# Performance work log

Measured on AMD Instinct MI355X. Metric: run time of the kernel, lower is better.

The kernel has to match this reference:

```python
import jax, jax.numpy as jnp
import numpy as np

N = 50000      # nodes
E = 640000     # edges
F_IN = 128     # in_channels
H = 128        # hidden / layer size
G = 64         # graphs in batch
OUT = 5        # classes


def _lin_init(key, fan_in, fan_out):
    s = 1.0 / np.sqrt(fan_in)
    kw, kb = jax.random.split(key)
    w = jax.random.uniform(kw, (fan_in, fan_out), jnp.float32, -s, s)
    b = jax.random.uniform(kb, (fan_out,), jnp.float32, -s, s)
    return w, b


def setup_inputs() -> dict:
    key = jax.random.key(0)
    ks = jax.random.split(key, 8)
    x = jax.random.normal(ks[0], (N, F_IN), jnp.float32)
    edge_index = jax.random.randint(ks[1], (2, E), 0, N, dtype=jnp.int64)
    # sorted graph assignment, every graph nonempty (sorted_randint-style)
    batch = (jnp.arange(N, dtype=jnp.int64) * G) // N
    c0w1, c0b1 = _lin_init(ks[2], F_IN, H)
    c0w2, c0b2 = _lin_init(ks[3], H, H)
    c1w1, c1b1 = _lin_init(ks[4], H, H)
    c1w2, c1b2 = _lin_init(ks[5], H, H)
    lw, lb = _lin_init(ks[6], H, OUT)
    return {"x": x, "edge_index": edge_index, "batch": batch,
            "conv0_w1": c0w1, "conv0_b1": c0b1, "conv0_w2": c0w2, "conv0_b2": c0b2,
            "conv1_w1": c1w1, "conv1_b1": c1b1, "conv1_w2": c1w2, "conv1_b2": c1b2,
            "lin_w": lw, "lin_b": lb}


def reference(x, edge_index, batch,
              conv0_w1, conv0_b1, conv0_w2, conv0_b2,
              conv1_w1, conv1_b1, conv1_w2, conv1_b2,
              lin_w, lin_b):
    src, dst = edge_index[0], edge_index[1]

    def gin_conv(h, w1, b1, w2, b2):
        # scatter-add neighbor aggregation: out_i = sum_{(j->i) in E} h_j
        agg = jax.ops.segment_sum(h[src], dst, num_segments=N)
        z = agg + h  # GIN with eps = 0 (train_eps=False)
        # PyG MLP (2 layers, eval mode): Linear -> ReLU -> Linear
        z = jax.nn.relu(z @ w1 + b1) @ w2 + b2
        return jax.nn.relu(z)  # outer .relu() in forward

    h = gin_conv(x, conv0_w1, conv0_b1, conv0_w2, conv0_b2)
    h = gin_conv(h, conv1_w1, conv1_b1, conv1_w2, conv1_b2)
    # global max pool over each graph (all segments nonempty by construction)
    pooled = jax.ops.segment_max(h, batch, num_segments=G)
    # dropout p=0.3 is a no-op in eval mode
    return pooled @ lin_w + lin_b
```

## Files before the change

### kernel.cpp

```cpp
#include <hip/hip_runtime.h>
#include <hip/hip_bf16.h>

#define N_NODES 50000
#define N_EDGES 640000
#define HDIM 128
#define NGRAPH 64
#define NOUT 5
#define CAP 64
#define POOL_CH 16

typedef __attribute__((ext_vector_type(4))) short short4v;
typedef __attribute__((ext_vector_type(8))) short short8v;
typedef __attribute__((ext_vector_type(4))) float float4v;

__device__ inline float blo(unsigned u) { return __uint_as_float(u << 16); }
__device__ inline float bhi(unsigned u) { return __uint_as_float(u & 0xffff0000u); }
__device__ inline unsigned short f2b(float f) {
    __hip_bfloat16 h = __float2bfloat16(f);
    return *reinterpret_cast<unsigned short*>(&h);
}


__global__ void k_scatter_b(const int* __restrict__ src, const int* __restrict__ dst,
                            int* __restrict__ cur, int* __restrict__ adj) {
    int e = blockIdx.x * blockDim.x + threadIdx.x;
    if (e < N_EDGES) {
        int d = dst[e];
        int pos = atomicAdd(&cur[d], 1);
        adj[(size_t)d * CAP + pos] = src[e];
    }
}

__global__ __launch_bounds__(256) void k_prep(const float* __restrict__ x,
                                              const float* __restrict__ w0a,
                                              const float* __restrict__ w0b,
                                              const float* __restrict__ w1a,
                                              const float* __restrict__ w1b,
                                              int* __restrict__ zero_p, int nz,
                                              unsigned short* __restrict__ wf,
                                              unsigned short* __restrict__ xb) {
    int i = blockIdx.x * 256 + threadIdx.x;
    if (i < nz) zero_p[i] = 0;
    if (i < 4 * 2048) {
        int m = i >> 11, rem = i & 2047;
        int c = rem >> 8, ks = (rem >> 6) & 3, lane = rem & 63;
        int r = lane & 15, g = lane >> 4;
        int n = c * 16 + r, k0 = ks * 32 + 4 * g;
        const float* w = (m == 0) ? w0a : (m == 1) ? w0b : (m == 2) ? w1a : w1b;
        unsigned short v[8];
#pragma unroll
        for (int j = 0; j < 4; j++) {
            v[j]     = f2b(w[(k0 + j) * HDIM + n]);
            v[4 + j] = f2b(w[(k0 + 16 + j) * HDIM + n]);
        }
        uint4 o;
        o.x = v[0] | ((unsigned)v[1] << 16);
        o.y = v[2] | ((unsigned)v[3] << 16);
        o.z = v[4] | ((unsigned)v[5] << 16);
        o.w = v[6] | ((unsigned)v[7] << 16);
        ((uint4*)wf)[i] = o;
    }
    if (i < N_NODES * 16) {
        int row = i >> 4;
        int p0 = (i & 15) * 8;
        int ks = p0 >> 5, g2 = (p0 >> 3) & 3;
        const float* xr = x + (size_t)row * HDIM + ks * 32 + 4 * g2;
        float4 a = *(const float4*)xr;
        float4 b = *(const float4*)(xr + 16);
        uint4 o;
        o.x = f2b(a.x) | ((unsigned)f2b(a.y) << 16);
        o.y = f2b(a.z) | ((unsigned)f2b(a.w) << 16);
        o.z = f2b(b.x) | ((unsigned)f2b(b.y) << 16);
        o.w = f2b(b.z) | ((unsigned)f2b(b.w) << 16);
        *(uint4*)&xb[(size_t)row * HDIM + p0] = o;
    }
}

__global__ __launch_bounds__(256) void k_agg_b(const unsigned short* __restrict__ h,
                                               const int* __restrict__ cnt,
                                               const int* __restrict__ adj,
                                               unsigned short* __restrict__ out) {
    int node = blockIdx.x * 16 + (threadIdx.x >> 4);
    if (node >= N_NODES) return;
    int c = (threadIdx.x & 15) * 8;
    const unsigned short* hc = h + c;
    uint4 sv = *(const uint4*)(hc + (size_t)node * HDIM);
    float acc[8];
    acc[0] = blo(sv.x); acc[1] = bhi(sv.x);
    acc[2] = blo(sv.y); acc[3] = bhi(sv.y);
    acc[4] = blo(sv.z); acc[5] = bhi(sv.z);
    acc[6] = blo(sv.w); acc[7] = bhi(sv.w);
#define ACC8(v) do { \
        acc[0] += blo(v.x); acc[1] += bhi(v.x); \
        acc[2] += blo(v.y); acc[3] += bhi(v.y); \
        acc[4] += blo(v.z); acc[5] += bhi(v.z); \
        acc[6] += blo(v.w); acc[7] += bhi(v.w); } while (0)
    int s = node * CAP;
    int e = s + cnt[node];
    int k = s;
    for (; k + 4 <= e; k += 4) {
        int j0 = adj[k], j1 = adj[k + 1], j2 = adj[k + 2], j3 = adj[k + 3];
        uint4 v0 = *(const uint4*)(hc + (size_t)j0 * HDIM);
        uint4 v1 = *(const uint4*)(hc + (size_t)j1 * HDIM);
        uint4 v2 = *(const uint4*)(hc + (size_t)j2 * HDIM);
        uint4 v3 = *(const uint4*)(hc + (size_t)j3 * HDIM);
        ACC8(v0); ACC8(v1); ACC8(v2); ACC8(v3);
    }
    for (; k < e; k++) {
        int j = adj[k];
        uint4 v = *(const uint4*)(hc + (size_t)j * HDIM);
        ACC8(v);
    }
#undef ACC8
    uint4 o;
    o.x = f2b(acc[0]) | ((unsigned)f2b(acc[1]) << 16);
    o.y = f2b(acc[2]) | ((unsigned)f2b(acc[3]) << 16);
    o.z = f2b(acc[4]) | ((unsigned)f2b(acc[5]) << 16);
    o.w = f2b(acc[6]) | ((unsigned)f2b(acc[7]) << 16);
    *(uint4*)&out[(size_t)node * HDIM + c] = o;
}

template <bool POOL>
__global__ __launch_bounds__(256, 2) void k_mlp(const unsigned short* __restrict__ A,
                                                const unsigned short* __restrict__ w1f,
                                                const unsigned short* __restrict__ w2f,
                                                const float* __restrict__ b1,
                                                const float* __restrict__ b2,
                                                unsigned short* __restrict__ C,
                                                unsigned* __restrict__ pooled) {
    __shared__ uint4 lw1[2048];
    __shared__ uint4 lw2[2048];
    int tid = threadIdx.x;
    int lane = tid & 63;
    int w = tid >> 6;
    int r = lane & 15;
    int g = lane >> 4;
    int row0 = blockIdx.x * 128 + w * 32 + r;

    short8v fbv[2][4];
#pragma unroll
    for (int rt = 0; rt < 2; rt++) {
        int row = row0 + rt * 16;
        int rowc = (row < N_NODES) ? row : (N_NODES - 1);
        const unsigned short* arow = A + (size_t)rowc * HDIM;
#pragma unroll
        for (int ks = 0; ks < 4; ks++)
            fbv[rt][ks] = *(const short8v*)(arow + ks * 32 + g * 8);
    }

    {
        const uint4* g1 = (const uint4*)w1f;
        const uint4* g2 = (const uint4*)w2f;
#pragma unroll
        for (int i = 0; i < 8; i++) lw1[tid + i * 256] = g1[tid + i * 256];
#pragma unroll
        for (int i = 0; i < 8; i++) lw2[tid + i * 256] = g2[tid + i * 256];
    }
    __syncthreads();

    float4v acc1[2][8];
#pragma unroll
    for (int rt = 0; rt < 2; rt++)
#pragma unroll
        for (int c = 0; c < 8; c++) acc1[rt][c] = (float4v){0.f, 0.f, 0.f, 0.f};
#pragma unroll
    for (int ks = 0; ks < 4; ks++)
#pragma unroll
        for (int c = 0; c < 8; c++) {
            short8v fa = *(const short8v*)&lw1[(c * 4 + ks) * 64 + lane];
#pragma unroll
            for (int rt = 0; rt < 2; rt++)
                acc1[rt][c] = __builtin_amdgcn_mfma_f32_16x16x32_bf16(fa, fbv[rt][ks], acc1[rt][c], 0, 0, 0);
        }

    short8v fb2[2][4];
#pragma unroll
    for (int ks = 0; ks < 4; ks++) {
        float4 bA = *(const float4*)&b1[(2 * ks) * 16 + 4 * g];
        float4 bB = *(const float4*)&b1[(2 * ks + 1) * 16 + 4 * g];
#pragma unroll
        for (int rt = 0; rt < 2; rt++) {
            short8v f;
            f[0] = (short)f2b(fmaxf(acc1[rt][2 * ks][0] + bA.x, 0.f));
            f[1] = (short)f2b(fmaxf(acc1[rt][2 * ks][1] + bA.y, 0.f));
            f[2] = (short)f2b(fmaxf(acc1[rt][2 * ks][2] + bA.z, 0.f));
            f[3] = (short)f2b(fmaxf(acc1[rt][2 * ks][3] + bA.w, 0.f));
            f[4] = (short)f2b(fmaxf(acc1[rt][2 * ks + 1][0] + bB.x, 0.f));
            f[5] = (short)f2b(fmaxf(acc1[rt][2 * ks + 1][1] + bB.y, 0.f));
            f[6] = (short)f2b(fmaxf(acc1[rt][2 * ks + 1][2] + bB.z, 0.f));
            f[7] = (short)f2b(fmaxf(acc1[rt][2 * ks + 1][3] + bB.w, 0.f));
            fb2[rt][ks] = f;
        }
    }

    float4v acc2[2][8];
#pragma unroll
    for (int rt = 0; rt < 2; rt++)
#pragma unroll
        for (int c = 0; c < 8; c++) acc2[rt][c] = (float4v){0.f, 0.f, 0.f, 0.f};
#pragma unroll
    for (int ks = 0; ks < 4; ks++)
#pragma unroll
        for (int c = 0; c < 8; c++) {
            short8v fa = *(const short8v*)&lw2[(c * 4 + ks) * 64 + lane];
#pragma unroll
            for (int rt = 0; rt < 2; rt++)
                acc2[rt][c] = __builtin_amdgcn_mfma_f32_16x16x32_bf16(fa, fb2[rt][ks], acc2[rt][c], 0, 0, 0);
        }

    if constexpr (!POOL) {
#pragma unroll
        for (int rt = 0; rt < 2; rt++) {
            int row = row0 + rt * 16;
            bool ok = (row < N_NODES);
#pragma unroll
            for (int ks = 0; ks < 4; ks++) {
                float4 bA = *(const float4*)&b2[ks * 32 + 4 * g];
                float4 bB = *(const float4*)&b2[ks * 32 + 16 + 4 * g];
                uint4 st;
                st.x = f2b(fmaxf(acc2[rt][2 * ks][0] + bA.x, 0.f)) |
                       ((unsigned)f2b(fmaxf(acc2[rt][2 * ks][1] + bA.y, 0.f)) << 16);
                st.y = f2b(fmaxf(acc2[rt][2 * ks][2] + bA.z, 0.f)) |
                       ((unsigned)f2b(fmaxf(acc2[rt][2 * ks][3] + bA.w, 0.f)) << 16);
                st.z = f2b(fmaxf(acc2[rt][2 * ks + 1][0] + bB.x, 0.f)) |
                       ((unsigned)f2b(fmaxf(acc2[rt][2 * ks + 1][1] + bB.y, 0.f)) << 16);
                st.w = f2b(fmaxf(acc2[rt][2 * ks + 1][2] + bB.z, 0.f)) |
                       ((unsigned)f2b(fmaxf(acc2[rt][2 * ks + 1][3] + bB.w, 0.f)) << 16);
                if (ok) *(uint4*)&C[(size_t)row * HDIM + ks * 32 + g * 8] = st;
            }
        }
    } else {
        int base = blockIdx.x * 128 + w * 32;
        unsigned gid0 = ((unsigned)base * 64u) / 50000u;
        unsigned gid1 = ((unsigned)(base + 31) * 64u) / 50000u;
        bool fast = (base + 31 < N_NODES) && (gid0 == gid1);
        if (fast) {
            float vm[8][4];
#pragma unroll
            for (int c = 0; c < 8; c++) {
                int ks = c >> 1, h2 = c & 1;
                float4 bv = *(const float4*)&b2[ks * 32 + h2 * 16 + 4 * g];
                float bb[4] = {bv.x, bv.y, bv.z, bv.w};
#pragma unroll
                for (int i = 0; i < 4; i++)
                    vm[c][i] = fmaxf(fmaxf(acc2[0][c][i] + bb[i], 0.f),
                                     fmaxf(acc2[1][c][i] + bb[i], 0.f));
            }
#pragma unroll
            for (int mask = 1; mask <= 8; mask <<= 1)
#pragma unroll
                for (int c = 0; c < 8; c++)
#pragma unroll
                    for (int i = 0; i < 4; i++)
                        vm[c][i] = fmaxf(vm[c][i], __shfl_xor(vm[c][i], mask));
            if (r == 0) {
                unsigned* pool = pooled + gid0 * HDIM;
#pragma unroll
                for (int c = 0; c < 8; c++) {
                    int p = (c >> 1) * 32 + g * 8 + (c & 1) * 4;
#pragma unroll
                    for (int i = 0; i < 4; i++)
                        atomicMax(&pool[p + i], __float_as_uint(vm[c][i]));
                }
            }
        } else {
#pragma unroll
            for (int rt = 0; rt < 2; rt++) {
                int row = row0 + rt * 16;
                if (row < N_NODES) {
                    unsigned gid = ((unsigned)row * 64u) / 50000u;
                    unsigned* pool = pooled + gid * HDIM;
#pragma unroll
                    for (int c = 0; c < 8; c++) {
                        int ks = c >> 1, h2 = c & 1;
                        float4 bv = *(const float4*)&b2[ks * 32 + h2 * 16 + 4 * g];
                        float bb[4] = {bv.x, bv.y, bv.z, bv.w};
                        int p = ks * 32 + g * 8 + h2 * 4;
#pragma unroll
                        for (int i = 0; i < 4; i++)
                            atomicMax(&pool[p + i],
                                      __float_as_uint(fmaxf(acc2[rt][c][i] + bb[i], 0.f)));
                    }
                }
            }
        }
    }
}

__global__ void k_final(const float* __restrict__ pooled, const float* __restrict__ lw,
                        const float* __restrict__ lb, float* __restrict__ out) {
    int t = threadIdx.x;
    if (t >= NGRAPH * NOUT) return;
    int g = t / NOUT, o = t % NOUT;
    float acc = lb[o];
    for (int p = 0; p < HDIM; p++) {
        int col = (p & 0x60) | ((p & 4) << 2) | ((p & 0x18) >> 1) | (p & 3);
        acc = fmaf(pooled[g * HDIM + p], lw[col * NOUT + o], acc);
    }
    out[t] = acc;
}

extern "C" void kernel_launch(void* const* d_in, const int* in_sizes, int n_in,
                              void* d_out, int out_size, void* d_ws, size_t ws_size,
                              hipStream_t stream) {
    const float* x    = (const float*)d_in[0];
    const int*   ei   = (const int*)d_in[1];
    const int*   srcv = ei;
    const int*   dstv = ei + N_EDGES;
    const float* c0w1 = (const float*)d_in[3];
    const float* c0b1 = (const float*)d_in[4];
    const float* c0w2 = (const float*)d_in[5];
    const float* c0b2 = (const float*)d_in[6];
    const float* c1w1 = (const float*)d_in[7];
    const float* c1b1 = (const float*)d_in[8];
    const float* c1w2 = (const float*)d_in[9];
    const float* c1b2 = (const float*)d_in[10];
    const float* lw   = (const float*)d_in[11];
    const float* lb   = (const float*)d_in[12];
    float* out = (float*)d_out;

    char* ws = (char*)d_ws;
    int* cur      = (int*)(ws);
    float* pooled = (float*)(cur + N_NODES);
    int* adj      = (int*)(ws + 1ull * 1024 * 1024);
    unsigned short* wf = (unsigned short*)(ws + 14ull * 1024 * 1024);
    unsigned short* xb = (unsigned short*)(ws + 17ull * 1024 * 1024);
    unsigned short* b0 = (unsigned short*)(ws + 30ull * 1024 * 1024);
    unsigned short* b1 = (unsigned short*)(ws + 43ull * 1024 * 1024);

    const int NZ  = N_NODES + NGRAPH * HDIM;
    const int NBE = (N_EDGES + 255) / 256;
    const int NBL = (N_NODES + 127) / 128;
    const int NBA = (N_NODES + 15) / 16;
    const int NBC = (N_NODES * 16 + 255) / 256;

    k_prep<<<NBC, 256, 0, stream>>>(x, c0w1, c0w2, c1w1, c1w2, cur, NZ, wf, xb);

    k_scatter_b<<<NBE, 256, 0, stream>>>(srcv, dstv, cur, adj);

    k_agg_b<<<NBA, 256, 0, stream>>>(xb, cur, adj, b0);
    k_mlp<false><<<NBL, 256, 0, stream>>>(b0, wf, wf + 16384, c0b1, c0b2, b1, nullptr);

    k_agg_b<<<NBA, 256, 0, stream>>>(b1, cur, adj, b0);
    k_mlp<true><<<NBL, 256, 0, stream>>>(b0, wf + 32768, wf + 49152, c1b1, c1b2,
                                         nullptr, (unsigned*)pooled);

    k_final<<<1, 320, 0, stream>>>(pooled, lw, lb, out);
}
```

Measured before the change: 246.0 us.

## Halve MLP tile rows, reuse one LDS weight buffer, add XCD block swizzle

The MLP kernel now processes 64 rows per block (16 per wave) instead of 128, and holds both weight matrices in a single 32KB LDS buffer loaded in two phases. Launch bounds move to 4 blocks per SM. The aim is to cut register and LDS pressure so occupancy rises. An XCD-aware block index swizzle is also added to the prep, aggregation and MLP kernels so neighbouring blocks share a die's L2. In exchange, each block reloads weights twice, adds an extra barrier, and launches twice as many blocks, each reading weights again.

After: 240.0 us. 2.4% less time.

```diff
diff --git a/kernel.cpp b/kernel.cpp
--- a/kernel.cpp
+++ b/kernel.cpp
@@ -7,7 +7,6 @@
 #define NGRAPH 64
 #define NOUT 5
 #define CAP 64
-#define POOL_CH 16
 
 typedef __attribute__((ext_vector_type(4))) short short4v;
 typedef __attribute__((ext_vector_type(8))) short short8v;
@@ -18,6 +17,12 @@
 __device__ inline unsigned short f2b(float f) {
     __hip_bfloat16 h = __float2bfloat16(f);
     return *reinterpret_cast<unsigned short*>(&h);
+}
+
+__device__ inline int xcd_swz(int bid, int n) {
+    int x = bid & 7, d = bid >> 3;
+    int q = n >> 3, rem = n & 7;
+    return (x < rem) ? x * (q + 1) + d : rem * (q + 1) + (x - rem) * q + d;
 }
 
 
@@ -39,7 +44,7 @@
                                               int* __restrict__ zero_p, int nz,
                                               unsigned short* __restrict__ wf,
                                               unsigned short* __restrict__ xb) {
-    int i = blockIdx.x * 256 + threadIdx.x;
+    int i = xcd_swz(blockIdx.x, gridDim.x) * 256 + threadIdx.x;
     if (i < nz) zero_p[i] = 0;
     if (i < 4 * 2048) {
         int m = i >> 11, rem = i & 2047;
@@ -80,7 +85,7 @@
                                                const int* __restrict__ cnt,
                                                const int* __restrict__ adj,
                                                unsigned short* __restrict__ out) {
-    int node = blockIdx.x * 16 + (threadIdx.x >> 4);
+    int node = xcd_swz(blockIdx.x, gridDim.x) * 16 + (threadIdx.x >> 4);
     if (node >= N_NODES) return;
     int c = (threadIdx.x & 15) * 8;
     const unsigned short* hc = h + c;
@@ -121,119 +126,107 @@
 }
 
 template <bool POOL>
-__global__ __launch_bounds__(256, 2) void k_mlp(const unsigned short* __restrict__ A,
+__global__ __launch_bounds__(256, 4) void k_mlp(const unsigned short* __restrict__ A,
                                                 const unsigned short* __restrict__ w1f,
                                                 const unsigned short* __restrict__ w2f,
                                                 const float* __restrict__ b1,
                                                 const float* __restrict__ b2,
                                                 unsigned short* __restrict__ C,
                                                 unsigned* __restrict__ pooled) {
-    __shared__ uint4 lw1[2048];
-    __shared__ uint4 lw2[2048];
+    __shared__ uint4 lw[2048];
     int tid = threadIdx.x;
     int lane = tid & 63;
     int w = tid >> 6;
     int r = lane & 15;
     int g = lane >> 4;
-    int row0 = blockIdx.x * 128 + w * 32 + r;
-
-    short8v fbv[2][4];
-#pragma unroll
-    for (int rt = 0; rt < 2; rt++) {
-        int row = row0 + rt * 16;
-        int rowc = (row < N_NODES) ? row : (N_NODES - 1);
+    int Lb = xcd_swz(blockIdx.x, gridDim.x);
+    int base = Lb * 64 + w * 16;
+    int row = base + r;
+    int rowc = (row < N_NODES) ? row : (N_NODES - 1);
+
+    short8v fbv[4];
+    {
         const unsigned short* arow = A + (size_t)rowc * HDIM;
 #pragma unroll
         for (int ks = 0; ks < 4; ks++)
-            fbv[rt][ks] = *(const short8v*)(arow + ks * 32 + g * 8);
+            fbv[ks] = *(const short8v*)(arow + ks * 32 + g * 8);
     }
 
     {
         const uint4* g1 = (const uint4*)w1f;
-        const uint4* g2 = (const uint4*)w2f;
-#pragma unroll
-        for (int i = 0; i < 8; i++) lw1[tid + i * 256] = g1[tid + i * 256];
-#pragma unroll
-        for (int i = 0; i < 8; i++) lw2[tid + i * 256] = g2[tid + i * 256];
+#pragma unroll
+        for (int i = 0; i < 8; i++) lw[tid + i * 256] = g1[tid + i * 256];
     }
     __syncthreads();
 
-    float4v acc1[2][8];
-#pragma unroll
-    for (int rt = 0; rt < 2; rt++)
-#pragma unroll
-        for (int c = 0; c < 8; c++) acc1[rt][c] = (float4v){0.f, 0.f, 0.f, 0.f};
+    float4v acc1[8];
+#pragma unroll
+    for (int c = 0; c < 8; c++) acc1[c] = (float4v){0.f, 0.f, 0.f, 0.f};
 #pragma unroll
     for (int ks = 0; ks < 4; ks++)
 #pragma unroll
         for (int c = 0; c < 8; c++) {
-            short8v fa = *(const short8v*)&lw1[(c * 4 + ks) * 64 + lane];
-#pragma unroll
-            for (int rt = 0; rt < 2; rt++)
-                acc1[rt][c] = __builtin_amdgcn_mfma_f32_16x16x32_bf16(fa, fbv[rt][ks], acc1[rt][c], 0, 0, 0);
-        }
-
-    short8v fb2[2][4];
+            short8v fa = *(const short8v*)&lw[(c * 4 + ks) * 64 + lane];
+            acc1[c] = __builtin_amdgcn_mfma_f32_16x16x32_bf16(fa, fbv[ks], acc1[c], 0, 0, 0);
+        }
+
+    short8v fb2[4];
 #pragma unroll
     for (int ks = 0; ks < 4; ks++) {
         float4 bA = *(const float4*)&b1[(2 * ks) * 16 + 4 * g];
         float4 bB = *(const float4*)&b1[(2 * ks + 1) * 16 + 4 * g];
-#pragma unroll
-        for (int rt = 0; rt < 2; rt++) {
-            short8v f;
-            f[0] = (short)f2b(fmaxf(acc1[rt][2 * ks][0] + bA.x, 0.f));
-            f[1] = (short)f2b(fmaxf(acc1[rt][2 * ks][1] + bA.y, 0.f));
-            f[2] = (short)f2b(fmaxf(acc1[rt][2 * ks][2] + bA.z, 0.f));
-            f[3] = (short)f2b(fmaxf(acc1[rt][2 * ks][3] + bA.w, 0.f));
-            f[4] = (short)f2b(fmaxf(acc1[rt][2 * ks + 1][0] + bB.x, 0.f));
-            f[5] = (short)f2b(fmaxf(acc1[rt][2 * ks + 1][1] + bB.y, 0.f));
-            f[6] = (short)f2b(fmaxf(acc1[rt][2 * ks + 1][2] + bB.z, 0.f));
-            f[7] = (short)f2b(fmaxf(acc1[rt][2 * ks + 1][3] + bB.w, 0.f));
-            fb2[rt][ks] = f;
-        }
-    }
-
-    float4v acc2[2][8];
-#pragma unroll
-    for (int rt = 0; rt < 2; rt++)
-#pragma unroll
-        for (int c = 0; c < 8; c++) acc2[rt][c] = (float4v){0.f, 0.f, 0.f, 0.f};
+        short8v f;
+        f[0] = (short)f2b(fmaxf(acc1[2 * ks][0] + bA.x, 0.f));
+        f[1] = (short)f2b(fmaxf(acc1[2 * ks][1] + bA.y, 0.f));
+        f[2] = (short)f2b(fmaxf(acc1[2 * ks][2] + bA.z, 0.f));
+        f[3] = (short)f2b(fmaxf(acc1[2 * ks][3] + bA.w, 0.f));
+        f[4] = (short)f2b(fmaxf(acc1[2 * ks + 1][0] + bB.x, 0.f));
+        f[5] = (short)f2b(fmaxf(acc1[2 * ks + 1][1] + bB.y, 0.f));
+        f[6] = (short)f2b(fmaxf(acc1[2 * ks + 1][2] + bB.z, 0.f));
+        f[7] = (short)f2b(fmaxf(acc1[2 * ks + 1][3] + bB.w, 0.f));
+        fb2[ks] = f;
+    }
+    __syncthreads();
+
+    {
+        const uint4* g2 = (const uint4*)w2f;
+#pragma unroll
+        for (int i = 0; i < 8; i++) lw[tid + i * 256] = g2[tid + i * 256];
+    }
+    __syncthreads();
+
+    float4v acc2[8];
+#pragma unroll
+    for (int c = 0; c < 8; c++) acc2[c] = (float4v){0.f, 0.f, 0.f, 0.f};
 #pragma unroll
     for (int ks = 0; ks < 4; ks++)
 #pragma unroll
         for (int c = 0; c < 8; c++) {
-            short8v fa = *(const short8v*)&lw2[(c * 4 + ks) * 64 + lane];
-#pragma unroll
-            for (int rt = 0; rt < 2; rt++)
-                acc2[rt][c] = __builtin_amdgcn_mfma_f32_16x16x32_bf16(fa, fb2[rt][ks], acc2[rt][c], 0, 0, 0);
+            short8v fa = *(const short8v*)&lw[(c * 4 + ks) * 64 + lane];
+            acc2[c] = __builtin_amdgcn_mfma_f32_16x16x32_bf16(fa, fb2[ks], acc2[c], 0, 0, 0);
         }
 
     if constexpr (!POOL) {
-#pragma unroll
-        for (int rt = 0; rt < 2; rt++) {
-            int row = row0 + rt * 16;
-            bool ok = (row < N_NODES);
-#pragma unroll
-            for (int ks = 0; ks < 4; ks++) {
-                float4 bA = *(const float4*)&b2[ks * 32 + 4 * g];
-                float4 bB = *(const float4*)&b2[ks * 32 + 16 + 4 * g];
-                uint4 st;
-                st.x = f2b(fmaxf(acc2[rt][2 * ks][0] + bA.x, 0.f)) |
-                       ((unsigned)f2b(fmaxf(acc2[rt][2 * ks][1] + bA.y, 0.f)) << 16);
-                st.y = f2b(fmaxf(acc2[rt][2 * ks][2] + bA.z, 0.f)) |
-                       ((unsigned)f2b(fmaxf(acc2[rt][2 * ks][3] + bA.w, 0.f)) << 16);
-                st.z = f2b(fmaxf(acc2[rt][2 * ks + 1][0] + bB.x, 0.f)) |
-                       ((unsigned)f2b(fmaxf(acc2[rt][2 * ks + 1][1] + bB.y, 0.f)) << 16);
-                st.w = f2b(fmaxf(acc2[rt][2 * ks + 1][2] + bB.z, 0.f)) |
-                       ((unsigned)f2b(fmaxf(acc2[rt][2 * ks + 1][3] + bB.w, 0.f)) << 16);
-                if (ok) *(uint4*)&C[(size_t)row * HDIM + ks * 32 + g * 8] = st;
-            }
+        bool ok = (row < N_NODES);
+#pragma unroll
+        for (int ks = 0; ks < 4; ks++) {
+            float4 bA = *(const float4*)&b2[ks * 32 + 4 * g];
+            float4 bB = *(const float4*)&b2[ks * 32 + 16 + 4 * g];
+            uint4 st;
+            st.x = f2b(fmaxf(acc2[2 * ks][0] + bA.x, 0.f)) |
+                   ((unsigned)f2b(fmaxf(acc2[2 * ks][1] + bA.y, 0.f)) << 16);
+            st.y = f2b(fmaxf(acc2[2 * ks][2] + bA.z, 0.f)) |
+                   ((unsigned)f2b(fmaxf(acc2[2 * ks][3] + bA.w, 0.f)) << 16);
+            st.z = f2b(fmaxf(acc2[2 * ks + 1][0] + bB.x, 0.f)) |
+                   ((unsigned)f2b(fmaxf(acc2[2 * ks + 1][1] + bB.y, 0.f)) << 16);
+            st.w = f2b(fmaxf(acc2[2 * ks + 1][2] + bB.z, 0.f)) |
+                   ((unsigned)f2b(fmaxf(acc2[2 * ks + 1][3] + bB.w, 0.f)) << 16);
+            if (ok) *(uint4*)&C[(size_t)row * HDIM + ks * 32 + g * 8] = st;
         }
     } else {
-        int base = blockIdx.x * 128 + w * 32;
         unsigned gid0 = ((unsigned)base * 64u) / 50000u;
-        unsigned gid1 = ((unsigned)(base + 31) * 64u) / 50000u;
-        bool fast = (base + 31 < N_NODES) && (gid0 == gid1);
+        unsigned gid1 = ((unsigned)(base + 15) * 64u) / 50000u;
+        bool fast = (base + 15 < N_NODES) && (gid0 == gid1);
         if (fast) {
             float vm[8][4];
 #pragma unroll
@@ -243,8 +236,7 @@
                 float bb[4] = {bv.x, bv.y, bv.z, bv.w};
 #pragma unroll
                 for (int i = 0; i < 4; i++)
-                    vm[c][i] = fmaxf(fmaxf(acc2[0][c][i] + bb[i], 0.f),
-                                     fmaxf(acc2[1][c][i] + bb[i], 0.f));
+                    vm[c][i] = fmaxf(acc2[c][i] + bb[i], 0.f);
             }
 #pragma unroll
             for (int mask = 1; mask <= 8; mask <<= 1)
@@ -263,25 +255,19 @@
                         atomicMax(&pool[p + i], __float_as_uint(vm[c][i]));
                 }
             }
-        } else {
-#pragma unroll
-            for (int rt = 0; rt < 2; rt++) {
-                int row = row0 + rt * 16;
-                if (row < N_NODES) {
-                    unsigned gid = ((unsigned)row * 64u) / 50000u;
-                    unsigned* pool = pooled + gid * HDIM;
-#pragma unroll
-                    for (int c = 0; c < 8; c++) {
-                        int ks = c >> 1, h2 = c & 1;
-                        float4 bv = *(const float4*)&b2[ks * 32 + h2 * 16 + 4 * g];
-                        float bb[4] = {bv.x, bv.y, bv.z, bv.w};
-                        int p = ks * 32 + g * 8 + h2 * 4;
-#pragma unroll
-                        for (int i = 0; i < 4; i++)
-                            atomicMax(&pool[p + i],
-                                      __float_as_uint(fmaxf(acc2[rt][c][i] + bb[i], 0.f)));
-                    }
-                }
+        } else if (row < N_NODES) {
+            unsigned gid = ((unsigned)row * 64u) / 50000u;
+            unsigned* pool = pooled + gid * HDIM;
+#pragma unroll
+            for (int c = 0; c < 8; c++) {
+                int ks = c >> 1, h2 = c & 1;
+                float4 bv = *(const float4*)&b2[ks * 32 + h2 * 16 + 4 * g];
+                float bb[4] = {bv.x, bv.y, bv.z, bv.w};
+                int p = ks * 32 + g * 8 + h2 * 4;
+#pragma unroll
+                for (int i = 0; i < 4; i++)
+                    atomicMax(&pool[p + i],
+                              __float_as_uint(fmaxf(acc2[c][i] + bb[i], 0.f)));
             }
         }
     }
@@ -330,7 +316,7 @@
 
     const int NZ  = N_NODES + NGRAPH * HDIM;
     const int NBE = (N_EDGES + 255) / 256;
-    const int NBL = (N_NODES + 127) / 128;
+    const int NBL = (N_NODES + 63) / 64;
     const int NBA = (N_NODES + 15) / 16;
     const int NBC = (N_NODES * 16 + 255) / 256;
 
```
